# Kernel tuning notes

Hardware: AMD Instinct MI355X
Metric: run time of the kernel (lower is better)

Reference implementation:

```python
import jax, jax.numpy as jnp
import numpy as np

B, P, H, W = 8, 128, 32, 32
NC = 4                 # num_classes = NUM_REL_GROUP + 1
DOBJ = 4424            # 2*DOBJ = 8848
CIN = 256
C = 128 + 8848         # 8976 GCN channel dim


def setup_inputs() -> dict:
    key = jax.random.key(0)
    ks = jax.random.split(key, 24)
    s = 0.02  # weight scale to keep activations moderate
    inp = {
        "x": jax.random.normal(ks[0], (B, CIN, H, W), jnp.float32),
        "rel_pair_idxs": jax.random.randint(ks[1], (B, P, 2), 0, 640, dtype=jnp.int32),
        "obj_rep": jax.random.normal(ks[2], (640, DOBJ), jnp.float32),
        # ADD_GCN params
        "fc_w": jax.random.normal(ks[3], (NC, CIN), jnp.float32) * s,
        "ct_w": jax.random.normal(ks[4], (128, CIN), jnp.float32) * s,
        "ct_b": jnp.zeros((128,), jnp.float32),
        # DynamicGraphConvolution params
        "A": jax.random.normal(ks[5], (NC, NC), jnp.float32) * 0.25,          # static_adj conv1d (no bias)
        "sw_w": jax.random.normal(ks[6], (C, C), jnp.float32) * s / np.sqrt(C) * 30,
        "sw_b": jnp.zeros((C,), jnp.float32),
        "cg_w": jax.random.normal(ks[7], (C, C), jnp.float32) * s / np.sqrt(C) * 30,
        "cg_b": jnp.zeros((C,), jnp.float32),
        "bn_g": jnp.ones((C,), jnp.float32),
        "bn_b": jnp.zeros((C,), jnp.float32),
        "bn_m": jnp.zeros((C,), jnp.float32),
        "bn_v": jnp.ones((C,), jnp.float32),
        "co_w": jax.random.normal(ks[8], (NC, 2 * C), jnp.float32) * s / np.sqrt(C) * 30,
        "co_b": jnp.zeros((NC,), jnp.float32),
        "dw_w": jax.random.normal(ks[9], (C, C), jnp.float32) * s / np.sqrt(C) * 30,
        "dw_b": jnp.zeros((C,), jnp.float32),
        "ll_w": jax.random.normal(ks[10], (NC, C), jnp.float32) * s / np.sqrt(C) * 30,
        "ll_b": jnp.zeros((NC,), jnp.float32),
        "mask_mat": jnp.eye(NC, dtype=jnp.float32),
    }
    return inp


def reference(x, rel_pair_idxs, obj_rep, fc_w, ct_w, ct_b, A, sw_w, sw_b,
              cg_w, cg_b, bn_g, bn_b, bn_m, bn_v, co_w, co_b, dw_w, dw_b,
              ll_w, ll_b, mask_mat):
    leaky = lambda t: jax.nn.leaky_relu(t, 0.2)
    b, cin, h, w = x.shape
    xr = x.reshape(b, cin, h * w)                                  # (B,256,HW)

    # forward_classification_sm: fc -> topk(1).mean == max over spatial
    y = jnp.einsum('oc,bcs->bos', fc_w, xr)                        # (B,NC,HW)
    out1 = y.max(-1)                                               # (B,NC)

    # forward_sam
    mask = jax.nn.sigmoid(y)                                       # (B,NC,HW)
    v = jnp.einsum('oc,bcs->bos', ct_w, xr) + ct_b[None, :, None]  # (B,128,HW)
    v = jnp.einsum('bcs,bns->bcn', v, mask)                        # (B,128,NC)

    # pairwise object features (gather), tiled over NC node slots
    o1 = obj_rep[rel_pair_idxs[..., 0]]                            # (B,P,DOBJ)
    o2 = obj_rep[rel_pair_idxs[..., 1]]
    pf = jnp.concatenate([o1, o2], -1)                             # (B,P,8848)
    p = pf.shape[1]
    pf = jnp.broadcast_to(pf[..., None], pf.shape + (NC,))         # (B,P,8848,NC)
    vb = jnp.broadcast_to(v[:, None], (b, p) + v.shape[1:])        # (B,P,128,NC)
    g = jnp.concatenate([pf, vb], 2).reshape(b * p, C, NC)         # (BP,C,NC)

    # --- DynamicGraphConvolution ---
    # static GCN: node-mix conv1d (no bias) + leaky, then channel 1x1 conv + leaky
    xs = leaky(jnp.einsum('nm,pcm->pcn', A, g))                    # (BP,C,NC)
    xs = leaky(jnp.einsum('oc,pcn->pon', sw_w, xs) + sw_b[None, :, None])
    hg = g + xs

    # dynamic adjacency
    glb = hg.mean(-1)                                              # (BP,C) gap
    glb = glb @ cg_w.T + cg_b                                      # conv_global (1x1)
    glb = (glb - bn_m) * jax.lax.rsqrt(bn_v + 1e-5) * bn_g + bn_b  # BN (eval)
    glb = leaky(glb)
    # conv_create_co_mat over cat([glb_expand, hg], ch) without materializing cat
    adj = jax.nn.sigmoid(
        jnp.einsum('oc,pc->po', co_w[:, :C], glb)[:, :, None]
        + jnp.einsum('oc,pcn->pon', co_w[:, C:], hg)
        + co_b[None, :, None])                                     # (BP,NC,NC)

    # dynamic GCN
    hd = leaky(jnp.einsum('pcn,pnm->pcm', hg, adj))
    z = leaky(jnp.einsum('oc,pcn->pon', dw_w, hd) + dw_b[None, :, None])  # (BP,C,NC)

    # head: last_linear + leaky, masked diagonal sum
    out2 = leaky(jnp.einsum('oc,pcn->pon', ll_w, z) + ll_b[None, :, None])  # (BP,NC,NC)
    out2 = (out2 * jax.lax.stop_gradient(mask_mat)).sum(-1)        # (BP,NC)

    o1b = jnp.broadcast_to(out1[:, None], (b, p, NC)).reshape(b * p, NC)
    return ((o1b + out2) * 0.5).reshape(b, p, NC)
```

## Files before the change

### kernel.cpp

```cpp
#include <hip/hip_runtime.h>
#include <stdint.h>

#define DEVI __device__ __forceinline__

typedef unsigned short u16;
typedef __bf16 bf16x8 __attribute__((ext_vector_type(8)));
typedef float f32x4 __attribute__((ext_vector_type(4)));
typedef u16 u16x8 __attribute__((ext_vector_type(8)));

DEVI u16 f2bf(float f){
  union { float f; unsigned u; } v; v.f = f;
  unsigned r = v.u + 0x7FFFu + ((v.u >> 16) & 1u);
  return (u16)(r >> 16);
}
DEVI float bf2f(u16 h){
  union { unsigned u; float f; } v; v.u = ((unsigned)h) << 16;
  return v.f;
}
DEVI float lky(float t){ return t > 0.f ? t : 0.2f * t; }

#define GLD16(gp, lp) __builtin_amdgcn_global_load_lds( \
    (const __attribute__((address_space(1))) void*)(gp), \
    (__attribute__((address_space(3))) void*)(lp), 16, 0, 0)


DEVI void stage_half(const u16* __restrict__ G, size_t grow0, int kcol, int Kp,
                     u16* lds, int t)
{
  #pragma unroll
  for (int j = 0; j < 2; ++j){
    const int off16 = j*512 + t;
    const int rl = off16 >> 3, sl = off16 & 7;
    const u16* gp = G + (grow0 + rl)*(size_t)Kp + kcol + ((sl ^ (rl & 7))*8);
    GLD16(gp, lds + off16*8);
  }
}

template<int RB, int RA>
DEVI void ph_reads(const u16* __restrict__ Ab, const u16* __restrict__ Bb,
                   bf16x8 (&afr)[4][2], bf16x8 (&bfr)[4][2],
                   int wr, int wc, int l4, int l15)
{
  if constexpr (RA >= 0){
    #pragma unroll
    for (int m = 0; m < 4; ++m){
      const int r = wr*128 + RA*64 + m*16 + l15;
      afr[m][0] = *(const bf16x8*)&Ab[r*64 + (((0+l4) ^ (r & 7))*8)];
      afr[m][1] = *(const bf16x8*)&Ab[r*64 + (((4+l4) ^ (r & 7))*8)];
    }
  }
  if constexpr (RB >= 0){
    #pragma unroll
    for (int nn = 0; nn < 2; ++nn){
      const int r = wc*64 + (RB+nn)*16 + l15;
      bfr[RB+nn][0] = *(const bf16x8*)&Bb[r*64 + (((0+l4) ^ (r & 7))*8)];
      bfr[RB+nn][1] = *(const bf16x8*)&Bb[r*64 + (((4+l4) ^ (r & 7))*8)];
    }
  }
}

template<int MH, int NH, int VM>
DEVI void ph_mfma(bf16x8 (&afr)[4][2], bf16x8 (&bfr)[4][2], f32x4 (&acc)[8][4])
{
  __builtin_amdgcn_s_barrier();
  asm volatile("s_waitcnt lgkmcnt(0)" ::: "memory");
  __builtin_amdgcn_sched_barrier(0);
  __builtin_amdgcn_s_setprio(1);
  #pragma unroll
  for (int m = 0; m < 4; ++m)
    #pragma unroll
    for (int nn = 0; nn < 2; ++nn)
      #pragma unroll
      for (int ks = 0; ks < 2; ++ks)
        acc[MH*4+m][NH+nn] = __builtin_amdgcn_mfma_f32_16x16x32_bf16(
            afr[m][ks], bfr[NH+nn][ks], acc[MH*4+m][NH+nn], 0, 0, 0);
  __builtin_amdgcn_s_setprio(0);
  if constexpr (VM == 4){
    __builtin_amdgcn_sched_barrier(0);
    asm volatile("s_waitcnt vmcnt(4)" ::: "memory");
  }
  __builtin_amdgcn_s_barrier();
}

template<int EPI>
__global__ __launch_bounds__(512, 2)
void gemm256(const u16* __restrict__ A, const u16* __restrict__ B,
             int Kp, int Nt, int SN, int Mreal, float* __restrict__ C, long long ldc,
             const float* __restrict__ bias, const float* __restrict__ scale,
             const float* __restrict__ off, const float* __restrict__ llw,
             float* __restrict__ oacc)
{
  __shared__ __align__(16) u16 As[2][16384];
  __shared__ __align__(16) u16 Bs[2][16384];
  const int t    = threadIdx.x;
  const int lane = t & 63;
  const int wid  = t >> 6;
  const int wr = wid >> 2, wc = wid & 3;
  const int l4 = lane >> 4, l15 = lane & 15;

  const int nwg = gridDim.x;
  const int xc = blockIdx.x & 7, pp = blockIdx.x >> 3;
  const int qq = nwg >> 3, rr = nwg & 7;
  const int wg = (xc < rr ? xc*(qq+1) : rr*(qq+1) + (xc-rr)*qq) + pp;
  const int strip_sz = (nwg / Nt) * SN;
  const int strip = wg / strip_sz, srem = wg % strip_sz;
  const int mt = srem / SN, nt = strip*SN + srem % SN;

  const size_t am0 = (size_t)mt*256;
  const size_t bn0 = (size_t)nt*256;

  f32x4 acc[8][4];
  #pragma unroll
  for (int i = 0; i < 8; ++i)
    #pragma unroll
    for (int j = 0; j < 4; ++j) acc[i][j] = f32x4{0.f,0.f,0.f,0.f};
  bf16x8 afr[4][2], bfr[4][2];

  const int NT2 = Kp >> 6;
  const int NI  = NT2 >> 1;

  stage_half(A, am0+0,   0,  Kp, &As[0][0],    t);
  stage_half(A, am0+128, 0,  Kp, &As[0][8192], t);
  stage_half(B, bn0+0,   0,  Kp, &Bs[0][0],    t);
  stage_half(B, bn0+128, 0,  Kp, &Bs[0][8192], t);
  stage_half(B, bn0+0,   64, Kp, &Bs[1][0],    t);
  stage_half(B, bn0+128, 64, Kp, &Bs[1][8192], t);
  asm volatile("s_waitcnt vmcnt(4)" ::: "memory");
  __builtin_amdgcn_s_barrier();

  for (int i = 0; i < NI; ++i){
    const int k1  = 2*i + 1;
    const int ts0 = (2*i+2 < NT2) ? 2*i+2 : 2*i;
    const int ts1 = (2*i+3 < NT2) ? 2*i+3 : 2*i+1;
    ph_reads<0,0>(&As[0][0], &Bs[0][0], afr, bfr, wr, wc, l4, l15);
    stage_half(A, am0+0,   k1*64,  Kp, &As[1][0],    t);
    ph_mfma<0,0,-1>(afr, bfr, acc);
    ph_reads<2,-1>(&As[0][0], &Bs[0][0], afr, bfr, wr, wc, l4, l15);
    stage_half(A, am0+128, k1*64,  Kp, &As[1][8192], t);
    ph_mfma<0,2,-1>(afr, bfr, acc);
    ph_reads<-1,1>(&As[0][0], &Bs[0][0], afr, bfr, wr, wc, l4, l15);
    stage_half(B, bn0+0,   ts0*64, Kp, &Bs[0][0],    t);
    ph_mfma<1,2,-1>(afr, bfr, acc);
    stage_half(B, bn0+128, ts0*64, Kp, &Bs[0][8192], t);
    ph_mfma<1,0,4>(afr, bfr, acc);
    ph_reads<0,0>(&As[1][0], &Bs[1][0], afr, bfr, wr, wc, l4, l15);
    stage_half(A, am0+0,   ts0*64, Kp, &As[0][0],    t);
    ph_mfma<0,0,-1>(afr, bfr, acc);
    ph_reads<2,-1>(&As[1][0], &Bs[1][0], afr, bfr, wr, wc, l4, l15);
    stage_half(A, am0+128, ts0*64, Kp, &As[0][8192], t);
    ph_mfma<0,2,-1>(afr, bfr, acc);
    ph_reads<-1,1>(&As[1][0], &Bs[1][0], afr, bfr, wr, wc, l4, l15);
    stage_half(B, bn0+0,   ts1*64, Kp, &Bs[1][0],    t);
    ph_mfma<1,2,-1>(afr, bfr, acc);
    stage_half(B, bn0+128, ts1*64, Kp, &Bs[1][8192], t);
    ph_mfma<1,0,4>(afr, bfr, acc);
  }
  asm volatile("s_waitcnt vmcnt(0)" ::: "memory");

  const int ob0 = mt*256 + wr*128;
  const int nb0 = nt*256 + wc*64;

  if (EPI == 0){
    #pragma unroll
    for (int mi = 0; mi < 8; ++mi){
      const int ob = ob0 + mi*16 + l4*4;
      if (ob < Mreal){
        #pragma unroll
        for (int ni = 0; ni < 4; ++ni){
          const int n = nb0 + ni*16 + l15;
          *(f32x4*)&C[(size_t)n*ldc + ob] = acc[mi][ni];
        }
      }
    }
  } else if (EPI == 2){
    #pragma unroll
    for (int mi = 0; mi < 8; ++mi){
      const int ob = ob0 + mi*16 + l4*4;
      if (ob < Mreal){
        const float sc0=scale[ob],sc1=scale[ob+1],sc2=scale[ob+2],sc3=scale[ob+3];
        const float of0=off[ob],of1=off[ob+1],of2=off[ob+2],of3=off[ob+3];
        #pragma unroll
        for (int ni = 0; ni < 4; ++ni){
          const int n = nb0 + ni*16 + l15;
          f32x4 a = acc[mi][ni];
          f32x4 vv = { lky(a[0]*sc0+of0), lky(a[1]*sc1+of1),
                       lky(a[2]*sc2+of2), lky(a[3]*sc3+of3) };
          *(f32x4*)&C[(size_t)n*ldc + ob] = vv;
        }
      }
    }
  } else {
    #pragma unroll
    for (int ni = 0; ni < 4; ++ni){
      float s0=0.f, s1=0.f, s2=0.f, s3=0.f;
      #pragma unroll
      for (int mi = 0; mi < 8; ++mi){
        #pragma unroll
        for (int r = 0; r < 4; ++r){
          const int o = ob0 + mi*16 + l4*4 + r;
          if (o < Mreal){
            const float val = lky(acc[mi][ni][r] + bias[o]);
            s0 += llw[o]         * val;
            s1 += llw[8976 + o]  * val;
            s2 += llw[17952 + o] * val;
            s3 += llw[26928 + o] * val;
          }
        }
      }
      const int n = nb0 + ni*16 + l15;
      const int q = n >> 2, m = n & 3;
      float sv[4] = {s0,s1,s2,s3};
      #pragma unroll
      for (int o4 = 0; o4 < 4; ++o4){
        float tt = sv[o4];
        tt += __shfl_xor(tt, 16);
        tt += __shfl_xor(tt, 32);
        if (l4 == 0) atomicAdd(&oacc[(q*4 + o4)*4 + m], tt);
      }
    }
  }
}

__global__ __launch_bounds__(256)
void gemm_vpre(const u16* __restrict__ A, const u16* __restrict__ B,
               int Kp, int Nt, int Mreal, float* __restrict__ C, long long ldc,
               const float* __restrict__ bias)
{
  __shared__ __align__(16) u16 As[2][4096];
  __shared__ __align__(16) u16 Bs[2][4096];
  const int tid  = threadIdx.x;
  const int lane = tid & 63;
  const int wr   = (tid >> 6) >> 1, wc = (tid >> 6) & 1;
  const int l4   = lane >> 4, l15 = lane & 15;
  const int mt   = blockIdx.x / Nt, nt = blockIdx.x % Nt;

  const size_t arow = (size_t)(mt*128 + (tid>>2)) * Kp + (tid&3)*8;
  const size_t brow = (size_t)(nt*128 + (tid>>2)) * Kp + (tid&3)*8;
  const int    ldst = (tid>>2)*32 + (tid&3)*8;
  const size_t rowskip = (size_t)64 * Kp;

  f32x4 acc[4][4];
  #pragma unroll
  for (int i=0;i<4;i++)
    #pragma unroll
    for (int j=0;j<4;j++) acc[i][j] = f32x4{0.f,0.f,0.f,0.f};

  const int NT = Kp >> 5;
  {
    const u16* a0 = A + arow; const u16* b0 = B + brow;
    GLD16(a0,           &As[0][ldst]);
    GLD16(a0 + rowskip, &As[0][ldst + 2048]);
    GLD16(b0,           &Bs[0][ldst]);
    GLD16(b0 + rowskip, &Bs[0][ldst + 2048]);
  }
  __syncthreads();

  for (int kt=0; kt<NT; ++kt){
    const int cur = kt & 1;
    if (kt + 1 < NT){
      const u16* a0 = A + arow + (size_t)(kt+1)*32;
      const u16* b0 = B + brow + (size_t)(kt+1)*32;
      GLD16(a0,           &As[cur^1][ldst]);
      GLD16(a0 + rowskip, &As[cur^1][ldst + 2048]);
      GLD16(b0,           &Bs[cur^1][ldst]);
      GLD16(b0 + rowskip, &Bs[cur^1][ldst + 2048]);
    }
    bf16x8 af[4], bf[4];
    #pragma unroll
    for (int mi=0;mi<4;mi++)
      af[mi] = *(const bf16x8*)&As[cur][(wr*64 + mi*16 + l15)*32 + l4*8];
    #pragma unroll
    for (int ni=0;ni<4;ni++)
      bf[ni] = *(const bf16x8*)&Bs[cur][(wc*64 + ni*16 + l15)*32 + l4*8];
    #pragma unroll
    for (int mi=0;mi<4;mi++)
      #pragma unroll
      for (int ni=0;ni<4;ni++)
        acc[mi][ni] = __builtin_amdgcn_mfma_f32_16x16x32_bf16(af[mi], bf[ni], acc[mi][ni], 0, 0, 0);
    __syncthreads();
  }

  const int ob0 = mt*128 + wr*64;
  const int nb0 = nt*128 + wc*64;
  #pragma unroll
  for (int mi=0;mi<4;mi++)
    #pragma unroll
    for (int r=0;r<4;r++){
      const int o = ob0 + mi*16 + l4*4 + r;
      if (o < Mreal){
        const float bb = bias[o];
        #pragma unroll
        for (int ni=0;ni<4;ni++){
          const int n = nb0 + ni*16 + l15;
          C[(size_t)o*ldc + n] = acc[mi][ni][r] + bb;
        }
      }
    }
}

__global__ void k_cvt_pad(const float* __restrict__ src, int srows, int scols,
                          int lds_, int koff, u16* __restrict__ dst, int Kp)
{
  const int r = blockIdx.x;
  const int nch = Kp >> 3;
  for (int ch = threadIdx.x; ch < nch; ch += blockDim.x){
    const int k = ch*8;
    u16 o[8];
    if (r < srows){
      #pragma unroll
      for (int i=0;i<8;i++){
        const int kk = k + i;
        o[i] = (kk < scols) ? f2bf(src[(size_t)r*lds_ + koff + kk]) : (u16)0;
      }
    } else {
      #pragma unroll
      for (int i=0;i<8;i++) o[i] = 0;
    }
    u16x8 vv = { o[0],o[1],o[2],o[3],o[4],o[5],o[6],o[7] };
    *(u16x8*)&dst[(size_t)r*Kp + k] = vv;
  }
}

__global__ void k_cvt_obj(const float* __restrict__ obj, u16* __restrict__ dst)
{
  const int r = blockIdx.x;
  const int ab = (r >= 640);
  const float* src = obj + (size_t)(ab ? r-640 : r)*4424;
  for (int ch = threadIdx.x; ch < 560; ch += 256){
    const int k = ch*8;
    u16 o[8];
    #pragma unroll
    for (int i=0;i<8;i++){
      const int kk = k+i;
      float f = (kk < 4424) ? src[kk] : 0.f;
      if (ab) f = fabsf(f);
      o[i] = f2bf(f);
    }
    u16x8 vv = { o[0],o[1],o[2],o[3],o[4],o[5],o[6],o[7] };
    *(u16x8*)&dst[(size_t)r*4480 + k] = vv;
  }
}

__global__ void k_xT(const float* __restrict__ x, u16* __restrict__ xT)
{
  __shared__ float t[32][33];
  const int bid = blockIdx.x;
  const int b = bid >> 8; const int cs = (bid >> 5) & 7; const int ss = bid & 31;
  const int tx = threadIdx.x & 31, ty = threadIdx.x >> 5;
  #pragma unroll
  for (int i=0;i<4;i++){
    const int r = ty + i*8;
    t[r][tx] = x[((size_t)(b*256 + cs*32 + r))*1024 + ss*32 + tx];
  }
  __syncthreads();
  #pragma unroll
  for (int i=0;i<4;i++){
    const int r = ty + i*8;
    xT[((size_t)(b*1024 + ss*32 + r))*256 + cs*32 + tx] = f2bf(t[tx][r]);
  }
}

__global__ void k_ymask(const float* __restrict__ x, const float* __restrict__ fcw,
                        float* __restrict__ y, float* __restrict__ mask)
{
  __shared__ float fc[1024];
  const int b = blockIdx.x >> 2, st = blockIdx.x & 3;
  for (int i=threadIdx.x; i<1024; i+=256) fc[i] = fcw[i];
  __syncthreads();
  const int s = st*256 + threadIdx.x;
  float a0=0,a1=0,a2=0,a3=0;
  for (int c=0;c<256;c++){
    const float xv = x[((size_t)(b*256+c))*1024 + s];
    a0 += fc[c]*xv; a1 += fc[256+c]*xv; a2 += fc[512+c]*xv; a3 += fc[768+c]*xv;
  }
  const size_t base = (size_t)(b*4)*1024 + s;
  y[base]        = a0; mask[base]        = 1.f/(1.f+expf(-a0));
  y[base+1024]   = a1; mask[base+1024]   = 1.f/(1.f+expf(-a1));
  y[base+2048]   = a2; mask[base+2048]   = 1.f/(1.f+expf(-a2));
  y[base+3072]   = a3; mask[base+3072]   = 1.f/(1.f+expf(-a3));
}

__global__ void k_out1(const float* __restrict__ y, float* __restrict__ out1){
  const int bn = blockIdx.x;
  float m = -3.4e38f;
  for (int s=threadIdx.x; s<1024; s+=256) m = fmaxf(m, y[(size_t)bn*1024+s]);
  for (int o=32;o;o>>=1) m = fmaxf(m, __shfl_xor(m,o));
  __shared__ float red[4];
  if ((threadIdx.x&63)==0) red[threadIdx.x>>6] = m;
  __syncthreads();
  if (threadIdx.x==0) out1[bn] = fmaxf(fmaxf(red[0],red[1]),fmaxf(red[2],red[3]));
}

__global__ void k_v(const float* __restrict__ vpreT, const float* __restrict__ mask,
                    float* __restrict__ v){
  const int b = blockIdx.x >> 7, j = blockIdx.x & 127;
  float a[4]={0,0,0,0};
  for (int s=threadIdx.x; s<1024; s+=256){
    const float pv = vpreT[(size_t)j*8192 + b*1024 + s];
    #pragma unroll
    for (int m=0;m<4;m++) a[m] += pv * mask[((size_t)(b*4+m))*1024 + s];
  }
  __shared__ float red[4][5];
  #pragma unroll
  for (int m=0;m<4;m++){
    float t=a[m];
    for (int o=32;o;o>>=1) t += __shfl_xor(t,o);
    if ((threadIdx.x&63)==0) red[m][threadIdx.x>>6]=t;
  }
  __syncthreads();
  if (threadIdx.x<4)
    v[(size_t)(b*128+j)*4 + threadIdx.x] =
      red[threadIdx.x][0]+red[threadIdx.x][1]+red[threadIdx.x][2]+red[threadIdx.x][3];
}

__global__ void k_lv(const float* __restrict__ Am, const float* __restrict__ v,
                     float* __restrict__ lv){
  const int idx = blockIdx.x*256 + threadIdx.x;
  if (idx < 1024){
    #pragma unroll
    for (int n=0;n<4;n++){
      float s=0;
      #pragma unroll
      for (int m=0;m<4;m++) s += Am[n*4+m]*v[idx*4+m];
      lv[idx*4+n] = lky(s);
    }
  }
}

__global__ void k_sV(const float* __restrict__ sw, const float* __restrict__ lv,
                     float* __restrict__ sV){
  __shared__ float l[4096];
  for (int i=threadIdx.x; i<4096; i+=256) l[i]=lv[i];
  __syncthreads();
  const int o = blockIdx.x*256 + threadIdx.x;
  if (o >= 8976) return;
  float acc[8][4] = {};
  const float* row = sw + (size_t)o*8976 + 8848;
  for (int j=0;j<128;j++){
    const float wv = row[j];
    #pragma unroll
    for (int b=0;b<8;b++){
      const float* lb = &l[(b*128+j)*4];
      #pragma unroll
      for (int n=0;n<4;n++) acc[b][n] += wv*lb[n];
    }
  }
  #pragma unroll
  for (int b=0;b<8;b++){
    f32x4 vv = {acc[b][0],acc[b][1],acc[b][2],acc[b][3]};
    *(f32x4*)&sV[((size_t)b*8976 + o)*4] = vv;
  }
}

__global__ void k_so(const float* __restrict__ cgb, const float* __restrict__ g,
                     const float* __restrict__ b2, const float* __restrict__ m,
                     const float* __restrict__ vvar, float* __restrict__ so){
  const int o = blockIdx.x*256+threadIdx.x;
  if (o<8976){
    const float sc = g[o]*rsqrtf(vvar[o]+1e-5f);
    so[o]=sc; so[8976+o] = (cgb[o]-m[o])*sc + b2[o];
  }
}

__global__ void k_glb_t2(const float* __restrict__ U, const float* __restrict__ obj,
                         const int* __restrict__ rel,
                         const float* __restrict__ sV, const float* __restrict__ swb,
                         const float* __restrict__ v, const float* __restrict__ Am,
                         const float* __restrict__ cow, u16* __restrict__ glbB,
                         float* __restrict__ t2)
{
  const int q = blockIdx.x; const int b = q >> 7;
  const int i1 = rel[q*2], i2 = rel[q*2+1];
  const float* u1  = U + (size_t)i1*17952;
  const float* u2  = U + (size_t)i2*17952 + 8976;
  const float* u1a = U + (size_t)(640+i1)*17952;
  const float* u2a = U + (size_t)(640+i2)*17952 + 8976;
  const float* o1 = obj + (size_t)i1*4424;
  const float* o2 = obj + (size_t)i2*4424;
  float rA[4], aA[4];
  #pragma unroll
  for (int n=0;n<4;n++){
    const float s = Am[n*4]+Am[n*4+1]+Am[n*4+2]+Am[n*4+3];
    rA[n]=0.6f*s; aA[n]=0.4f*fabsf(s);
  }
  float t2a[16] = {};
  for (int c = threadIdx.x; c < 9088; c += 256){
    if (c < 8976){
      const float p1 = u1[c] + u2[c];
      const float p2 = u1a[c] + u2a[c];
      const f32x4 sv = *(const f32x4*)&sV[((size_t)b*8976 + c)*4];
      const float sb = swb[c];
      const float gs = (c < 4424) ? o1[c] : (c < 8848) ? o2[c-4424] : 0.f;
      float hg[4]; float sum = 0.f;
      #pragma unroll
      for (int n=0;n<4;n++){
        const float xs2 = lky(rA[n]*p1 + aA[n]*p2 + sv[n] + sb);
        const float g = (c < 8848) ? gs : v[((size_t)b*128 + (c-8848))*4 + n];
        hg[n] = g + xs2; sum += hg[n];
      }
      glbB[(size_t)q*9088 + c] = f2bf(0.25f*sum);
      #pragma unroll
      for (int o4=0;o4<4;o4++){
        const float cw = cow[(size_t)o4*17952 + 8976 + c];
        #pragma unroll
        for (int n=0;n<4;n++) t2a[o4*4+n] += cw*hg[n];
      }
    } else {
      glbB[(size_t)q*9088 + c] = 0;
    }
  }
  __shared__ float red[16][5];
  #pragma unroll
  for (int i=0;i<16;i++){
    float t = t2a[i];
    for (int o=32;o;o>>=1) t += __shfl_xor(t,o);
    if ((threadIdx.x&63)==0) red[i][threadIdx.x>>6]=t;
  }
  __syncthreads();
  if (threadIdx.x < 16)
    t2[q*16+threadIdx.x] = red[threadIdx.x][0]+red[threadIdx.x][1]
                          +red[threadIdx.x][2]+red[threadIdx.x][3];
}

__global__ void k_adj(const float* __restrict__ glb2, const float* __restrict__ cow,
                      const float* __restrict__ t2, const float* __restrict__ cob,
                      float* __restrict__ adj)
{
  const int q = blockIdx.x;
  float a[4]={0,0,0,0};
  for (int c=threadIdx.x; c<8976; c+=256){
    const float g = glb2[(size_t)q*8976+c];
    #pragma unroll
    for (int o=0;o<4;o++) a[o] += cow[(size_t)o*17952 + c]*g;
  }
  __shared__ float red[4][5]; __shared__ float co1[4];
  #pragma unroll
  for (int i=0;i<4;i++){
    float t=a[i]; for (int o=32;o;o>>=1) t += __shfl_xor(t,o);
    if ((threadIdx.x&63)==0) red[i][threadIdx.x>>6]=t;
  }
  __syncthreads();
  if (threadIdx.x<4)
    co1[threadIdx.x]=red[threadIdx.x][0]+red[threadIdx.x][1]+red[threadIdx.x][2]+red[threadIdx.x][3];
  __syncthreads();
  if (threadIdx.x<16){
    const int a_=threadIdx.x>>2, m=threadIdx.x&3;
    const float t = co1[a_] + t2[q*16 + a_*4 + m] + cob[a_];
    adj[q*16 + a_*4 + m] = 1.f/(1.f+expf(-t));
  }
}

__global__ void k_hd(const float* __restrict__ U, const float* __restrict__ obj,
                     const int* __restrict__ rel,
                     const float* __restrict__ sV, const float* __restrict__ swb,
                     const float* __restrict__ v, const float* __restrict__ Am,
                     const float* __restrict__ adj, u16* __restrict__ hdb)
{
  const int q = blockIdx.x; const int b = q>>7;
  const int i1 = rel[q*2], i2 = rel[q*2+1];
  const float* u1  = U + (size_t)i1*17952;
  const float* u2  = U + (size_t)i2*17952 + 8976;
  const float* u1a = U + (size_t)(640+i1)*17952;
  const float* u2a = U + (size_t)(640+i2)*17952 + 8976;
  const float* o1 = obj + (size_t)i1*4424;
  const float* o2 = obj + (size_t)i2*4424;
  float rA[4], aA[4];
  #pragma unroll
  for (int n=0;n<4;n++){
    const float s = Am[n*4]+Am[n*4+1]+Am[n*4+2]+Am[n*4+3];
    rA[n]=0.6f*s; aA[n]=0.4f*fabsf(s);
  }
  __shared__ float aj[16];
  if (threadIdx.x<16) aj[threadIdx.x] = adj[q*16+threadIdx.x];
  __syncthreads();
  float ajr[16];
  #pragma unroll
  for (int i=0;i<16;i++) ajr[i]=aj[i];
  for (int c=threadIdx.x; c<9088; c+=256){
    if (c<8976){
      const float p1 = u1[c] + u2[c];
      const float p2 = u1a[c] + u2a[c];
      const f32x4 sv = *(const f32x4*)&sV[((size_t)b*8976 + c)*4];
      const float sb = swb[c];
      const float gs = (c < 4424) ? o1[c] : (c < 8848) ? o2[c-4424] : 0.f;
      float hg[4];
      #pragma unroll
      for (int n=0;n<4;n++){
        const float xs2 = lky(rA[n]*p1 + aA[n]*p2 + sv[n] + sb);
        const float g = (c < 8848) ? gs : v[((size_t)b*128 + (c-8848))*4 + n];
        hg[n] = g + xs2;
      }
      #pragma unroll
      for (int m=0;m<4;m++){
        const float hv = lky(hg[0]*ajr[m] + hg[1]*ajr[4+m] + hg[2]*ajr[8+m] + hg[3]*ajr[12+m]);
        hdb[((size_t)(q*4+m))*9088 + c] = f2bf(hv);
      }
    } else {
      #pragma unroll
      for (int m=0;m<4;m++) hdb[((size_t)(q*4+m))*9088 + c] = 0;
    }
  }
}

__global__ void k_final(const float* __restrict__ o2f, const float* __restrict__ out1,
                        const float* __restrict__ llb, const float* __restrict__ mm,
                        float* __restrict__ out)
{
  const int idx = blockIdx.x*256+threadIdx.x;
  if (idx < 4096){
    const int q = idx>>2, o = idx&3, b = q>>7;
    float s=0.f;
    #pragma unroll
    for (int m=0;m<4;m++) s += lky(o2f[(q*4+o)*4+m] + llb[o]) * mm[o*4+m];
    out[idx] = 0.5f*(out1[b*4+o] + s);
  }
}

extern "C" void kernel_launch(void* const* d_in, const int* in_sizes, int n_in,
                              void* d_out, int out_size, void* d_ws, size_t ws_size,
                              hipStream_t stream)
{
  const float* x    = (const float*)d_in[0];
  const int*   rel  = (const int*)d_in[1];
  const float* obj  = (const float*)d_in[2];
  const float* fcw  = (const float*)d_in[3];
  const float* ctw  = (const float*)d_in[4];
  const float* ctb  = (const float*)d_in[5];
  const float* Am   = (const float*)d_in[6];
  const float* sww  = (const float*)d_in[7];
  const float* swb  = (const float*)d_in[8];
  const float* cgw  = (const float*)d_in[9];
  const float* cgb  = (const float*)d_in[10];
  const float* bng  = (const float*)d_in[11];
  const float* bnb  = (const float*)d_in[12];
  const float* bnm  = (const float*)d_in[13];
  const float* bnv  = (const float*)d_in[14];
  const float* cow  = (const float*)d_in[15];
  const float* cob  = (const float*)d_in[16];
  const float* dww  = (const float*)d_in[17];
  const float* dwb  = (const float*)d_in[18];
  const float* llw  = (const float*)d_in[19];
  const float* llb  = (const float*)d_in[20];
  const float* mm   = (const float*)d_in[21];
  float* out = (float*)d_out;
  (void)in_sizes; (void)n_in; (void)out_size; (void)ws_size;

  char* ws = (char*)d_ws;
  size_t off = 0;
  auto alloc = [&](size_t bytes)->char*{
    char* p = ws + off; off = (off + bytes + 255) & ~(size_t)255; return p;
  };
  u16*   Wb    = (u16*)  alloc((size_t)9216*9088*2);
  float* U     = (float*)alloc((size_t)1280*17952*4);
  u16*   glbB  = (u16*)  alloc((size_t)1024*9088*2);
  u16*   hdb   = (u16*)  alloc((size_t)4096*9088*2);
  u16*   objB  = (u16*)  alloc((size_t)1280*4480*2);
  float* glb2  = (float*)alloc((size_t)1024*8976*4);
  u16*   xT    = (u16*)  alloc((size_t)8192*256*2);
  u16*   ctwb  = (u16*)  alloc((size_t)128*256*2);
  float* y     = (float*)alloc((size_t)32768*4);
  float* mask  = (float*)alloc((size_t)32768*4);
  float* out1  = (float*)alloc((size_t)32*4);
  float* vpreT = (float*)alloc((size_t)128*8192*4);
  float* v     = (float*)alloc((size_t)4096*4);
  float* lv    = (float*)alloc((size_t)4096*4);
  float* sV    = (float*)alloc((size_t)287232*4);
  float* so    = (float*)alloc((size_t)2*8976*4);
  float* t2    = (float*)alloc((size_t)16384*4);
  float* adj   = (float*)alloc((size_t)16384*4);
  float* o2f   = (float*)alloc((size_t)16384*4);

  k_xT<<<dim3(2048), dim3(256), 0, stream>>>(x, xT);
  k_cvt_pad<<<dim3(128), dim3(256), 0, stream>>>(ctw, 128, 256, 256, 0, ctwb, 256);
  k_ymask<<<dim3(32), dim3(256), 0, stream>>>(x, fcw, y, mask);
  k_out1<<<dim3(32), dim3(256), 0, stream>>>(y, out1);
  gemm_vpre<<<dim3(64), dim3(256), 0, stream>>>(
      ctwb, xT, 256, 64, 128, vpreT, (long long)8192, ctb);
  k_v<<<dim3(1024), dim3(256), 0, stream>>>(vpreT, mask, v);

  k_cvt_obj<<<dim3(1280), dim3(256), 0, stream>>>(obj, objB);
  k_cvt_pad<<<dim3(8976), dim3(256), 0, stream>>>(sww, 8976, 4424, 8976, 0, Wb, 4480);
  k_cvt_pad<<<dim3(9200), dim3(256), 0, stream>>>(sww, 8976, 4424, 8976, 4424,
                                                  Wb + (size_t)8976*4480, 4480);
  gemm256<0><<<dim3(71*5), dim3(512), 0, stream>>>(
      Wb, objB, 4480, 5, 5, 17952, U, (long long)17952,
      nullptr, nullptr, nullptr, nullptr, nullptr);

  k_lv<<<dim3(4), dim3(256), 0, stream>>>(Am, v, lv);
  k_sV<<<dim3(36), dim3(256), 0, stream>>>(sww, lv, sV);
  k_glb_t2<<<dim3(1024), dim3(256), 0, stream>>>(U, obj, rel, sV, swb, v, Am,
                                                 cow, glbB, t2);

  k_cvt_pad<<<dim3(9216), dim3(256), 0, stream>>>(cgw, 8976, 8976, 8976, 0, Wb, 9088);
  k_so<<<dim3(36), dim3(256), 0, stream>>>(cgb, bng, bnb, bnm, bnv, so);
  gemm256<2><<<dim3(36*4), dim3(512), 0, stream>>>(
      Wb, glbB, 9088, 4, 4, 8976, glb2, (long long)8976,
      nullptr, so, so + 8976, nullptr, nullptr);

  k_adj<<<dim3(1024), dim3(256), 0, stream>>>(glb2, cow, t2, cob, adj);
  k_cvt_pad<<<dim3(9216), dim3(256), 0, stream>>>(dww, 8976, 8976, 8976, 0, Wb, 9088);
  k_hd<<<dim3(1024), dim3(256), 0, stream>>>(U, obj, rel, sV, swb, v, Am, adj, hdb);

  hipMemsetAsync(o2f, 0, (size_t)16384*4, stream);
  gemm256<3><<<dim3(36*16), dim3(512), 0, stream>>>(
      Wb, hdb, 9088, 16, 8, 8976, nullptr, 0, dwb,
      nullptr, nullptr, llw, o2f);

  k_final<<<dim3(16), dim3(256), 0, stream>>>(o2f, out1, llb, mm, out);
}
```

Baseline: 2.112 ms.

## Overlap weight bf16 conversion with GEMMs using extra blocks and double-buffered weights

Adds extra workgroups to the first two GEMM launches. These blocks convert the next GEMM's fp32 weight matrix to padded bf16 in a second weight buffer while the GEMM blocks run. This removes the standalone conversion kernels from the critical path, provided the workspace is large enough for two weight buffers. It also drops the explicit lgkmcnt wait and sched_barriers in the MFMA phase, which gives the compiler more freedom but may weaken ordering of LDS reads. The conversion blocks compete with GEMM tiles for CUs and bandwidth.

```diff
diff --git a/kernel.cpp b/kernel.cpp
--- a/kernel.cpp
+++ b/kernel.cpp
@@ -63,8 +63,6 @@
 DEVI void ph_mfma(bf16x8 (&afr)[4][2], bf16x8 (&bfr)[4][2], f32x4 (&acc)[8][4])
 {
   __builtin_amdgcn_s_barrier();
-  asm volatile("s_waitcnt lgkmcnt(0)" ::: "memory");
-  __builtin_amdgcn_sched_barrier(0);
   __builtin_amdgcn_s_setprio(1);
   #pragma unroll
   for (int m = 0; m < 4; ++m)
@@ -76,7 +74,6 @@
             afr[m][ks], bfr[NH+nn][ks], acc[MH*4+m][NH+nn], 0, 0, 0);
   __builtin_amdgcn_s_setprio(0);
   if constexpr (VM == 4){
-    __builtin_amdgcn_sched_barrier(0);
     asm volatile("s_waitcnt vmcnt(4)" ::: "memory");
   }
   __builtin_amdgcn_s_barrier();
@@ -88,17 +85,45 @@
              int Kp, int Nt, int SN, int Mreal, float* __restrict__ C, long long ldc,
              const float* __restrict__ bias, const float* __restrict__ scale,
              const float* __restrict__ off, const float* __restrict__ llw,
-             float* __restrict__ oacc)
+             float* __restrict__ oacc,
+             int ngemm, const float* __restrict__ cvt_src, int cvt_srows,
+             int cvt_scols, int cvt_lstride, u16* __restrict__ cvt_dst,
+             int cvt_kp, int cvt_prows, int cvt_nblk)
 {
   __shared__ __align__(16) u16 As[2][16384];
   __shared__ __align__(16) u16 Bs[2][16384];
+
+  if ((int)blockIdx.x >= ngemm){
+    const int bid = blockIdx.x - ngemm;
+    const int nch = cvt_kp >> 3;
+    for (int r = bid; r < cvt_prows; r += cvt_nblk){
+      for (int ch = threadIdx.x; ch < nch; ch += 512){
+        const int k = ch*8;
+        u16 o[8];
+        if (r < cvt_srows){
+          #pragma unroll
+          for (int i=0;i<8;i++){
+            const int kk = k + i;
+            o[i] = (kk < cvt_scols) ? f2bf(cvt_src[(size_t)r*cvt_lstride + kk]) : (u16)0;
+          }
+        } else {
+          #pragma unroll
+          for (int i=0;i<8;i++) o[i] = 0;
+        }
+        u16x8 vv = { o[0],o[1],o[2],o[3],o[4],o[5],o[6],o[7] };
+        *(u16x8*)&cvt_dst[(size_t)r*cvt_kp + k] = vv;
+      }
+    }
+    return;
+  }
+
   const int t    = threadIdx.x;
   const int lane = t & 63;
   const int wid  = t >> 6;
   const int wr = wid >> 2, wc = wid & 3;
   const int l4 = lane >> 4, l15 = lane & 15;
 
-  const int nwg = gridDim.x;
+  const int nwg = ngemm;
   const int xc = blockIdx.x & 7, pp = blockIdx.x >> 3;
   const int qq = nwg >> 3, rr = nwg & 7;
   const int wg = (xc < rr ? xc*(qq+1) : rr*(qq+1) + (xc-rr)*qq) + pp;
@@ -643,14 +668,23 @@
   const float* llb  = (const float*)d_in[20];
   const float* mm   = (const float*)d_in[21];
   float* out = (float*)d_out;
-  (void)in_sizes; (void)n_in; (void)out_size; (void)ws_size;
-
+  (void)in_sizes; (void)n_in; (void)out_size;
+
+  const size_t WB = (size_t)9216*9088*2;
   char* ws = (char*)d_ws;
   size_t off = 0;
   auto alloc = [&](size_t bytes)->char*{
     char* p = ws + off; off = (off + bytes + 255) & ~(size_t)255; return p;
   };
-  u16*   Wb    = (u16*)  alloc((size_t)9216*9088*2);
+
+  const size_t SMALL = (size_t)91914240 + 18612224 + 74448896 + 11468800
+                     + 36765696 + 4194304 + 65536 + 131072 + 131072 + 256
+                     + 4194304 + 16384 + 16384 + 1148928 + 71808 + 65536*3
+                     + 64*1024;
+  const bool fused = (ws_size >= 2*WB + SMALL);
+
+  u16* WbA = (u16*)alloc(WB);
+  u16* WbB = fused ? (u16*)alloc(WB) : WbA;
   float* U     = (float*)alloc((size_t)1280*17952*4);
   u16*   glbB  = (u16*)  alloc((size_t)1024*9088*2);
   u16*   hdb   = (u16*)  alloc((size_t)4096*9088*2);
@@ -679,32 +713,51 @@
   k_v<<<dim3(1024), dim3(256), 0, stream>>>(vpreT, mask, v);
 
   k_cvt_obj<<<dim3(1280), dim3(256), 0, stream>>>(obj, objB);
-  k_cvt_pad<<<dim3(8976), dim3(256), 0, stream>>>(sww, 8976, 4424, 8976, 0, Wb, 4480);
+  k_cvt_pad<<<dim3(8976), dim3(256), 0, stream>>>(sww, 8976, 4424, 8976, 0, WbA, 4480);
   k_cvt_pad<<<dim3(9200), dim3(256), 0, stream>>>(sww, 8976, 4424, 8976, 4424,
-                                                  Wb + (size_t)8976*4480, 4480);
-  gemm256<0><<<dim3(71*5), dim3(512), 0, stream>>>(
-      Wb, objB, 4480, 5, 5, 17952, U, (long long)17952,
-      nullptr, nullptr, nullptr, nullptr, nullptr);
+                                                  WbA + (size_t)8976*4480, 4480);
+  if (fused){
+    gemm256<0><<<dim3(512), dim3(512), 0, stream>>>(
+        WbA, objB, 4480, 5, 5, 17952, U, (long long)17952,
+        nullptr, nullptr, nullptr, nullptr, nullptr,
+        355, cgw, 8976, 8976, 8976, WbB, 9088, 9216, 157);
+  } else {
+    gemm256<0><<<dim3(355), dim3(512), 0, stream>>>(
+        WbA, objB, 4480, 5, 5, 17952, U, (long long)17952,
+        nullptr, nullptr, nullptr, nullptr, nullptr,
+        355, nullptr, 0, 0, 0, nullptr, 8, 0, 1);
+  }
 
   k_lv<<<dim3(4), dim3(256), 0, stream>>>(Am, v, lv);
   k_sV<<<dim3(36), dim3(256), 0, stream>>>(sww, lv, sV);
   k_glb_t2<<<dim3(1024), dim3(256), 0, stream>>>(U, obj, rel, sV, swb, v, Am,
                                                  cow, glbB, t2);
 
-  k_cvt_pad<<<dim3(9216), dim3(256), 0, stream>>>(cgw, 8976, 8976, 8976, 0, Wb, 9088);
+  if (!fused)
+    k_cvt_pad<<<dim3(9216), dim3(256), 0, stream>>>(cgw, 8976, 8976, 8976, 0, WbB, 9088);
   k_so<<<dim3(36), dim3(256), 0, stream>>>(cgb, bng, bnb, bnm, bnv, so);
-  gemm256<2><<<dim3(36*4), dim3(512), 0, stream>>>(
-      Wb, glbB, 9088, 4, 4, 8976, glb2, (long long)8976,
-      nullptr, so, so + 8976, nullptr, nullptr);
+  if (fused){
+    gemm256<2><<<dim3(256), dim3(512), 0, stream>>>(
+        WbB, glbB, 9088, 4, 4, 8976, glb2, (long long)8976,
+        nullptr, so, so + 8976, nullptr, nullptr,
+        144, dww, 8976, 8976, 8976, WbA, 9088, 9216, 112);
+  } else {
+    gemm256<2><<<dim3(144), dim3(512), 0, stream>>>(
+        WbB, glbB, 9088, 4, 4, 8976, glb2, (long long)8976,
+        nullptr, so, so + 8976, nullptr, nullptr,
+        144, nullptr, 0, 0, 0, nullptr, 8, 0, 1);
+  }
 
   k_adj<<<dim3(1024), dim3(256), 0, stream>>>(glb2, cow, t2, cob, adj);
-  k_cvt_pad<<<dim3(9216), dim3(256), 0, stream>>>(dww, 8976, 8976, 8976, 0, Wb, 9088);
+  if (!fused)
+    k_cvt_pad<<<dim3(9216), dim3(256), 0, stream>>>(dww, 8976, 8976, 8976, 0, WbA, 9088);
   k_hd<<<dim3(1024), dim3(256), 0, stream>>>(U, obj, rel, sV, swb, v, Am, adj, hdb);
 
   hipMemsetAsync(o2f, 0, (size_t)16384*4, stream);
-  gemm256<3><<<dim3(36*16), dim3(512), 0, stream>>>(
-      Wb, hdb, 9088, 16, 8, 8976, nullptr, 0, dwb,
-      nullptr, nullptr, llw, o2f);
+  gemm256<3><<<dim3(576), dim3(512), 0, stream>>>(
+      WbA, hdb, 9088, 16, 8, 8976, nullptr, 0, dwb,
+      nullptr, nullptr, llw, o2f,
+      576, nullptr, 0, 0, 0, nullptr, 8, 0, 1);
 
   k_final<<<dim3(16), dim3(256), 0, stream>>>(o2f, out1, llb, mm, out);
 }
```

Result: no change. 2.142 ms (+1.4%).

## Triple-buffer A tiles in GEMM main loop and pad K to multiple of 384

Applied to the files above, without the earlier changes.

The GEMM now keeps three LDS buffers for the A operand, so A tiles are prefetched two k-steps ahead, and the loop is unrolled three-way with rotating buffers. The waitcnt depth goes from 4 to 8, and the explicit lgkmcnt wait and sched_barriers before the MFMAs are removed. K padding grows from 4480/9088 to 4608/9216 so the iteration count divides by three, which adds some zero-padded work and memory traffic. LDS use rises to 160KB per block, which may limit occupancy. Dropping the lgkmcnt(0) wait leaves it to the compiler to order LDS reads before the MFMAs that use them.

```diff
diff --git a/kernel.cpp b/kernel.cpp
--- a/kernel.cpp
+++ b/kernel.cpp
@@ -63,8 +63,6 @@
 DEVI void ph_mfma(bf16x8 (&afr)[4][2], bf16x8 (&bfr)[4][2], f32x4 (&acc)[8][4])
 {
   __builtin_amdgcn_s_barrier();
-  asm volatile("s_waitcnt lgkmcnt(0)" ::: "memory");
-  __builtin_amdgcn_sched_barrier(0);
   __builtin_amdgcn_s_setprio(1);
   #pragma unroll
   for (int m = 0; m < 4; ++m)
@@ -75,9 +73,8 @@
         acc[MH*4+m][NH+nn] = __builtin_amdgcn_mfma_f32_16x16x32_bf16(
             afr[m][ks], bfr[NH+nn][ks], acc[MH*4+m][NH+nn], 0, 0, 0);
   __builtin_amdgcn_s_setprio(0);
-  if constexpr (VM == 4){
-    __builtin_amdgcn_sched_barrier(0);
-    asm volatile("s_waitcnt vmcnt(4)" ::: "memory");
+  if constexpr (VM == 8){
+    asm volatile("s_waitcnt vmcnt(8)" ::: "memory");
   }
   __builtin_amdgcn_s_barrier();
 }
@@ -90,7 +87,7 @@
              const float* __restrict__ off, const float* __restrict__ llw,
              float* __restrict__ oacc)
 {
-  __shared__ __align__(16) u16 As[2][16384];
+  __shared__ __align__(16) u16 As[3][16384];
   __shared__ __align__(16) u16 Bs[2][16384];
   const int t    = threadIdx.x;
   const int lane = t & 63;
@@ -123,37 +120,44 @@
   stage_half(A, am0+128, 0,  Kp, &As[0][8192], t);
   stage_half(B, bn0+0,   0,  Kp, &Bs[0][0],    t);
   stage_half(B, bn0+128, 0,  Kp, &Bs[0][8192], t);
+  stage_half(A, am0+0,   64, Kp, &As[1][0],    t);
+  stage_half(A, am0+128, 64, Kp, &As[1][8192], t);
   stage_half(B, bn0+0,   64, Kp, &Bs[1][0],    t);
   stage_half(B, bn0+128, 64, Kp, &Bs[1][8192], t);
-  asm volatile("s_waitcnt vmcnt(4)" ::: "memory");
+  asm volatile("s_waitcnt vmcnt(8)" ::: "memory");
   __builtin_amdgcn_s_barrier();
 
-  for (int i = 0; i < NI; ++i){
-    const int k1  = 2*i + 1;
-    const int ts0 = (2*i+2 < NT2) ? 2*i+2 : 2*i;
-    const int ts1 = (2*i+3 < NT2) ? 2*i+3 : 2*i+1;
-    ph_reads<0,0>(&As[0][0], &Bs[0][0], afr, bfr, wr, wc, l4, l15);
-    stage_half(A, am0+0,   k1*64,  Kp, &As[1][0],    t);
+  auto ITER = [&](u16* Ae, u16* Ao, u16* S0, u16* S1, int i){
+    const int t2 = (2*i+2 < NT2) ? 2*i+2 : NT2-1;
+    const int t3 = (2*i+3 < NT2) ? 2*i+3 : NT2-1;
+    ph_reads<0,0>(Ae, &Bs[0][0], afr, bfr, wr, wc, l4, l15);
+    stage_half(A, am0+0,   t2*64, Kp, S0, t);
     ph_mfma<0,0,-1>(afr, bfr, acc);
-    ph_reads<2,-1>(&As[0][0], &Bs[0][0], afr, bfr, wr, wc, l4, l15);
-    stage_half(A, am0+128, k1*64,  Kp, &As[1][8192], t);
+    ph_reads<2,-1>(Ae, &Bs[0][0], afr, bfr, wr, wc, l4, l15);
+    stage_half(A, am0+128, t2*64, Kp, S0+8192, t);
     ph_mfma<0,2,-1>(afr, bfr, acc);
-    ph_reads<-1,1>(&As[0][0], &Bs[0][0], afr, bfr, wr, wc, l4, l15);
-    stage_half(B, bn0+0,   ts0*64, Kp, &Bs[0][0],    t);
+    ph_reads<-1,1>(Ae, &Bs[0][0], afr, bfr, wr, wc, l4, l15);
+    stage_half(B, bn0+0,   t2*64, Kp, &Bs[0][0], t);
     ph_mfma<1,2,-1>(afr, bfr, acc);
-    stage_half(B, bn0+128, ts0*64, Kp, &Bs[0][8192], t);
-    ph_mfma<1,0,4>(afr, bfr, acc);
-    ph_reads<0,0>(&As[1][0], &Bs[1][0], afr, bfr, wr, wc, l4, l15);
-    stage_half(A, am0+0,   ts0*64, Kp, &As[0][0],    t);
+    stage_half(B, bn0+128, t2*64, Kp, &Bs[0][8192], t);
+    ph_mfma<1,0,8>(afr, bfr, acc);
+    ph_reads<0,0>(Ao, &Bs[1][0], afr, bfr, wr, wc, l4, l15);
+    stage_half(A, am0+0,   t3*64, Kp, S1, t);
     ph_mfma<0,0,-1>(afr, bfr, acc);
-    ph_reads<2,-1>(&As[1][0], &Bs[1][0], afr, bfr, wr, wc, l4, l15);
-    stage_half(A, am0+128, ts0*64, Kp, &As[0][8192], t);
+    ph_reads<2,-1>(Ao, &Bs[1][0], afr, bfr, wr, wc, l4, l15);
+    stage_half(A, am0+128, t3*64, Kp, S1+8192, t);
     ph_mfma<0,2,-1>(afr, bfr, acc);
-    ph_reads<-1,1>(&As[1][0], &Bs[1][0], afr, bfr, wr, wc, l4, l15);
-    stage_half(B, bn0+0,   ts1*64, Kp, &Bs[1][0],    t);
+    ph_reads<-1,1>(Ao, &Bs[1][0], afr, bfr, wr, wc, l4, l15);
+    stage_half(B, bn0+0,   t3*64, Kp, &Bs[1][0], t);
     ph_mfma<1,2,-1>(afr, bfr, acc);
-    stage_half(B, bn0+128, ts1*64, Kp, &Bs[1][8192], t);
-    ph_mfma<1,0,4>(afr, bfr, acc);
+    stage_half(B, bn0+128, t3*64, Kp, &Bs[1][8192], t);
+    ph_mfma<1,0,8>(afr, bfr, acc);
+  };
+
+  for (int i = 0; i < NI; i += 3){
+    ITER(&As[0][0], &As[1][0], &As[2][0], &As[0][0], i);
+    ITER(&As[2][0], &As[0][0], &As[1][0], &As[2][0], i+1);
+    ITER(&As[1][0], &As[2][0], &As[0][0], &As[1][0], i+2);
   }
   asm volatile("s_waitcnt vmcnt(0)" ::: "memory");
 
@@ -326,7 +330,7 @@
   const int r = blockIdx.x;
   const int ab = (r >= 640);
   const float* src = obj + (size_t)(ab ? r-640 : r)*4424;
-  for (int ch = threadIdx.x; ch < 560; ch += 256){
+  for (int ch = threadIdx.x; ch < 576; ch += 256){
     const int k = ch*8;
     u16 o[8];
     #pragma unroll
@@ -337,7 +341,7 @@
       o[i] = f2bf(f);
     }
     u16x8 vv = { o[0],o[1],o[2],o[3],o[4],o[5],o[6],o[7] };
-    *(u16x8*)&dst[(size_t)r*4480 + k] = vv;
+    *(u16x8*)&dst[(size_t)r*4608 + k] = vv;
   }
 }
 
@@ -484,7 +488,7 @@
     rA[n]=0.6f*s; aA[n]=0.4f*fabsf(s);
   }
   float t2a[16] = {};
-  for (int c = threadIdx.x; c < 9088; c += 256){
+  for (int c = threadIdx.x; c < 9216; c += 256){
     if (c < 8976){
       const float p1 = u1[c] + u2[c];
       const float p2 = u1a[c] + u2a[c];
@@ -498,7 +502,7 @@
         const float g = (c < 8848) ? gs : v[((size_t)b*128 + (c-8848))*4 + n];
         hg[n] = g + xs2; sum += hg[n];
       }
-      glbB[(size_t)q*9088 + c] = f2bf(0.25f*sum);
+      glbB[(size_t)q*9216 + c] = f2bf(0.25f*sum);
       #pragma unroll
       for (int o4=0;o4<4;o4++){
         const float cw = cow[(size_t)o4*17952 + 8976 + c];
@@ -506,7 +510,7 @@
         for (int n=0;n<4;n++) t2a[o4*4+n] += cw*hg[n];
       }
     } else {
-      glbB[(size_t)q*9088 + c] = 0;
+      glbB[(size_t)q*9216 + c] = 0;
     }
   }
   __shared__ float red[16][5];
@@ -576,7 +580,7 @@
   float ajr[16];
   #pragma unroll
   for (int i=0;i<16;i++) ajr[i]=aj[i];
-  for (int c=threadIdx.x; c<9088; c+=256){
+  for (int c=threadIdx.x; c<9216; c+=256){
     if (c<8976){
       const float p1 = u1[c] + u2[c];
       const float p2 = u1a[c] + u2a[c];
@@ -593,11 +597,11 @@
       #pragma unroll
       for (int m=0;m<4;m++){
         const float hv = lky(hg[0]*ajr[m] + hg[1]*ajr[4+m] + hg[2]*ajr[8+m] + hg[3]*ajr[12+m]);
-        hdb[((size_t)(q*4+m))*9088 + c] = f2bf(hv);
+        hdb[((size_t)(q*4+m))*9216 + c] = f2bf(hv);
       }
     } else {
       #pragma unroll
-      for (int m=0;m<4;m++) hdb[((size_t)(q*4+m))*9088 + c] = 0;
+      for (int m=0;m<4;m++) hdb[((size_t)(q*4+m))*9216 + c] = 0;
     }
   }
 }
@@ -650,11 +654,11 @@
   auto alloc = [&](size_t bytes)->char*{
     char* p = ws + off; off = (off + bytes + 255) & ~(size_t)255; return p;
   };
-  u16*   Wb    = (u16*)  alloc((size_t)9216*9088*2);
+  u16*   Wb    = (u16*)  alloc((size_t)9216*9216*2);
   float* U     = (float*)alloc((size_t)1280*17952*4);
-  u16*   glbB  = (u16*)  alloc((size_t)1024*9088*2);
-  u16*   hdb   = (u16*)  alloc((size_t)4096*9088*2);
-  u16*   objB  = (u16*)  alloc((size_t)1280*4480*2);
+  u16*   glbB  = (u16*)  alloc((size_t)1024*9216*2);
+  u16*   hdb   = (u16*)  alloc((size_t)4096*9216*2);
+  u16*   objB  = (u16*)  alloc((size_t)1280*4608*2);
   float* glb2  = (float*)alloc((size_t)1024*8976*4);
   u16*   xT    = (u16*)  alloc((size_t)8192*256*2);
   u16*   ctwb  = (u16*)  alloc((size_t)128*256*2);
@@ -679,11 +683,11 @@
   k_v<<<dim3(1024), dim3(256), 0, stream>>>(vpreT, mask, v);
 
   k_cvt_obj<<<dim3(1280), dim3(256), 0, stream>>>(obj, objB);
-  k_cvt_pad<<<dim3(8976), dim3(256), 0, stream>>>(sww, 8976, 4424, 8976, 0, Wb, 4480);
+  k_cvt_pad<<<dim3(8976), dim3(256), 0, stream>>>(sww, 8976, 4424, 8976, 0, Wb, 4608);
   k_cvt_pad<<<dim3(9200), dim3(256), 0, stream>>>(sww, 8976, 4424, 8976, 4424,
-                                                  Wb + (size_t)8976*4480, 4480);
+                                                  Wb + (size_t)8976*4608, 4608);
   gemm256<0><<<dim3(71*5), dim3(512), 0, stream>>>(
-      Wb, objB, 4480, 5, 5, 17952, U, (long long)17952,
+      Wb, objB, 4608, 5, 5, 17952, U, (long long)17952,
       nullptr, nullptr, nullptr, nullptr, nullptr);
 
   k_lv<<<dim3(4), dim3(256), 0, stream>>>(Am, v, lv);
@@ -691,19 +695,19 @@
   k_glb_t2<<<dim3(1024), dim3(256), 0, stream>>>(U, obj, rel, sV, swb, v, Am,
                                                  cow, glbB, t2);
 
-  k_cvt_pad<<<dim3(9216), dim3(256), 0, stream>>>(cgw, 8976, 8976, 8976, 0, Wb, 9088);
+  k_cvt_pad<<<dim3(9216), dim3(256), 0, stream>>>(cgw, 8976, 8976, 8976, 0, Wb, 9216);
   k_so<<<dim3(36), dim3(256), 0, stream>>>(cgb, bng, bnb, bnm, bnv, so);
   gemm256<2><<<dim3(36*4), dim3(512), 0, stream>>>(
-      Wb, glbB, 9088, 4, 4, 8976, glb2, (long long)8976,
+      Wb, glbB, 9216, 4, 4, 8976, glb2, (long long)8976,
       nullptr, so, so + 8976, nullptr, nullptr);
 
   k_adj<<<dim3(1024), dim3(256), 0, stream>>>(glb2, cow, t2, cob, adj);
-  k_cvt_pad<<<dim3(9216), dim3(256), 0, stream>>>(dww, 8976, 8976, 8976, 0, Wb, 9088);
+  k_cvt_pad<<<dim3(9216), dim3(256), 0, stream>>>(dww, 8976, 8976, 8976, 0, Wb, 9216);
   k_hd<<<dim3(1024), dim3(256), 0, stream>>>(U, obj, rel, sV, swb, v, Am, adj, hdb);
 
   hipMemsetAsync(o2f, 0, (size_t)16384*4, stream);
   gemm256<3><<<dim3(36*16), dim3(512), 0, stream>>>(
-      Wb, hdb, 9088, 16, 8, 8976, nullptr, 0, dwb,
+      Wb, hdb, 9216, 16, 8, 8976, nullptr, 0, dwb,
       nullptr, nullptr, llw, o2f);
 
   k_final<<<dim3(16), dim3(256), 0, stream>>>(o2f, out1, llb, mm, out);
```

Result: slower. 2.278 ms (+7.9%).
